# Optimization experiments

Hardware: AMD Instinct MI355X
Metric: run time of the kernel (lower is better)

Reference implementation:

```python
import jax, jax.numpy as jnp
import numpy as np

B, T, V, NS, L, G, H = 16, 256, 18000, 30, 10, 3, 400


def setup_inputs() -> dict:
    key = jax.random.key(0)
    ks = jax.random.split(key, 12)
    return {
        'encoded_hidden': jax.random.normal(ks[0], (1, B, H), jnp.float32),
        'encoded_outputs': jax.random.normal(ks[1], (B, T, H), jnp.float32),
        'emb_weight': jax.random.normal(ks[2], (V, H), jnp.float32) * 0.02,
        'gru_w_ih': jax.random.normal(ks[3], (3 * H, H), jnp.float32) * 0.05,
        'gru_w_hh': jax.random.normal(ks[4], (3 * H, H), jnp.float32) * 0.05,
        'gru_b_ih': jnp.zeros((3 * H,), jnp.float32),
        'gru_b_hh': jnp.zeros((3 * H,), jnp.float32),
        'w_ratio': jax.random.normal(ks[5], (1, 3 * H), jnp.float32) * 0.05,
        'b_ratio': jnp.zeros((1,), jnp.float32),
        'w_gate': jax.random.normal(ks[6], (G, H), jnp.float32) * 0.05,
        'b_gate': jnp.zeros((G,), jnp.float32),
        'slot_emb': jax.random.normal(ks[7], (2 * NS, H), jnp.float32) * 0.1,
        'encoded_lens': jax.random.randint(ks[8], (B,), T // 2, T + 1, jnp.int32),
        'story': jax.random.randint(ks[9], (B, T), 0, V, jnp.int32),
        'target_batches': jax.random.randint(ks[10], (B, NS, L), 0, V, jnp.int32),
        'domain_idx': 2 * jnp.arange(NS, dtype=jnp.int32),
        'slotname_idx': 2 * jnp.arange(NS, dtype=jnp.int32) + 1,
    }


def _forward(encoded_hidden, encoded_outputs, emb_weight, gru_w_ih, gru_w_hh,
             gru_b_ih, gru_b_hh, w_ratio, b_ratio, w_gate, b_gate, slot_emb,
             encoded_lens, story, target_batches, domain_idx, slotname_idx):
    b, t, h = encoded_outputs.shape
    ns, l = target_batches.shape[1], target_batches.shape[2]
    n = ns * b  # flattened slot-major rows: row = slot*b + batch

    combined = slot_emb[domain_idx] + slot_emb[slotname_idx]          # (NS,H)
    dec_in0 = jnp.repeat(combined, b, axis=0)                          # (N,H)
    h0 = jnp.tile(encoded_hidden[0], (ns, 1))                          # (N,H)
    enc = jnp.tile(encoded_outputs, (ns, 1, 1))                        # (N,T,H)
    story_rep = jnp.tile(story, (ns, 1))                               # (N,T)
    lens_rep = jnp.tile(encoded_lens, ns)                              # (N,)
    mask = jnp.arange(t)[None, :] < lens_rep[:, None]                  # (N,T)
    rows = jnp.arange(n)[:, None]

    # teacher forcing: decoder input at step wi>=1 is emb of target at wi-1
    tgt = jnp.transpose(target_batches, (2, 1, 0)).reshape(l, n)       # (L,N)
    dec_inputs = jnp.concatenate([dec_in0[None], emb_weight[tgt[:-1]]], axis=0)

    def step(hid, x):
        gi = x @ gru_w_ih.T + gru_b_ih
        gh = hid @ gru_w_hh.T + gru_b_hh
        i_r, i_z, i_n = jnp.split(gi, 3, axis=-1)
        h_r, h_z, h_n = jnp.split(gh, 3, axis=-1)
        r = jax.nn.sigmoid(i_r + h_r)
        z = jax.nn.sigmoid(i_z + h_z)
        nn_ = jnp.tanh(i_n + r * h_n)
        h_new = (1.0 - z) * nn_ + z * hid                              # (N,H)
        # attend over encoder outputs
        scores = jnp.einsum('nh,nth->nt', h_new, enc)
        scores = jnp.where(mask, scores, -1e9)
        prob = jax.nn.softmax(scores, axis=1)                          # (N,T)
        context = jnp.einsum('nt,nth->nh', prob, enc)                  # (N,H)
        # vocab distribution
        p_vocab = jax.nn.softmax(h_new @ emb_weight.T, axis=1)         # (N,V)
        # pointer-generator mix
        p_gen_vec = jnp.concatenate([h_new, context, x], axis=-1)      # (N,3H)
        switch = jax.nn.sigmoid(p_gen_vec @ w_ratio.T + b_ratio)       # (N,1)
        p_ctx = jnp.zeros_like(p_vocab).at[rows, story_rep].add(prob)  # scatter-add
        final = (1.0 - switch) * p_ctx + switch * p_vocab              # (N,V)
        return h_new, (final, context)

    _, (finals, contexts) = jax.lax.scan(step, h0, dec_inputs)
    points = finals.reshape(l, ns, b, -1).transpose(1, 2, 0, 3)        # (NS,B,L,V)
    gates = (contexts[0] @ w_gate.T + b_gate).reshape(ns, b, -1)       # (NS,B,G)
    return points, gates


def reference(encoded_hidden, encoded_outputs, emb_weight, gru_w_ih, gru_w_hh,
              gru_b_ih, gru_b_hh, w_ratio, b_ratio, w_gate, b_gate, slot_emb,
              encoded_lens, story, target_batches, domain_idx, slotname_idx):
    return _forward(encoded_hidden, encoded_outputs, emb_weight, gru_w_ih,
                    gru_w_hh, gru_b_ih, gru_b_hh, w_ratio, b_ratio, w_gate,
                    b_gate, slot_emb, encoded_lens, story, target_batches,
                    domain_idx, slotname_idx)
```

## Files before the change

kernel.cpp:

```cpp
#include <hip/hip_runtime.h>
#include <hip/hip_bf16.h>

#define Bq 16
#define Tq 256
#define Vq 18000
#define NSq 30
#define Lq 10
#define Gq 3
#define Hq 400
#define Nq (NSq * Bq)
#define H3q (3 * Hq)
#define NKT 25
#define NGV 564
#define NGW 38
#define NGH 15
#define NPB 288
#define NPB_USED 282
#define NGHB 152

typedef __bf16 bf16;
typedef __bf16 bf16x4 __attribute__((ext_vector_type(4)));
typedef __bf16 bf16x8 __attribute__((ext_vector_type(8)));
typedef float floatx16 __attribute__((ext_vector_type(16)));

__global__ __launch_bounds__(256) void k_f2b4(
    const float* __restrict__ src, bf16* __restrict__ dst, const int n4)
{
    int i = blockIdx.x * 256 + threadIdx.x;
    if (i >= n4) return;
    const float4 v = ((const float4*)src)[i];
    bf16x4 o;
    o[0] = (bf16)v.x; o[1] = (bf16)v.y; o[2] = (bf16)v.z; o[3] = (bf16)v.w;
    ((bf16x4*)dst)[i] = o;
}

__global__ __launch_bounds__(256) void k_enct(
    const bf16* __restrict__ encb, bf16* __restrict__ encT)
{
    const int b = blockIdx.x;
    const int k0 = blockIdx.y * 32;
    const int t = threadIdx.x;
    const bf16* src = encb + ((size_t)(b * Tq + t)) * Hq + k0;
    #pragma unroll
    for (int j = 0; j < 32; ++j) {
        if (k0 + j < Hq)
            encT[((size_t)b * Hq + k0 + j) * Tq + t] = src[j];
    }
}

__global__ __launch_bounds__(256) void k_packf(
    const float* __restrict__ src, bf16* __restrict__ dst,
    const int ngroups, const int nrows)
{
    const int i = blockIdx.x * 256 + threadIdx.x;
    if (i >= ngroups * NKT * 64) return;
    const int lane = i & 63;
    const int kt = (i >> 6) % NKT;
    const int g = i / (NKT * 64);
    int row = g * 32 + (lane & 31);
    if (row >= nrows) row = nrows - 1;
    const int k0 = kt * 16 + (lane >> 5) * 8;
    const float* s = src + (size_t)row * Hq + k0;
    const float4 a = *(const float4*)s;
    const float4 c = *(const float4*)(s + 4);
    bf16x8 o;
    o[0] = (bf16)a.x; o[1] = (bf16)a.y; o[2] = (bf16)a.z; o[3] = (bf16)a.w;
    o[4] = (bf16)c.x; o[5] = (bf16)c.y; o[6] = (bf16)c.z; o[7] = (bf16)c.w;
    *(bf16x8*)(dst + (size_t)i * 8) = o;
}

__global__ __launch_bounds__(256) void k_xball(
    const float* __restrict__ slot_emb, const int* __restrict__ dom,
    const int* __restrict__ slo, const float* __restrict__ emb,
    const int* __restrict__ tgt, bf16* __restrict__ xbp,
    bf16* __restrict__ xlin)
{
    const int i = blockIdx.x * 256 + threadIdx.x;
    if (i >= Lq * NGH * NKT * 64) return;
    const int lane = i & 63;
    const int kt = (i >> 6) % NKT;
    const int gg = i / (NKT * 64);
    const int g = gg % NGH;
    const int s = gg / NGH;
    const int n = g * 32 + (lane & 31);
    const int slot = n >> 4, b = n & (Bq - 1);
    const int k0 = kt * 16 + (lane >> 5) * 8;
    float v[8];
    if (s == 0) {
        const float* p1 = slot_emb + (size_t)dom[slot] * Hq + k0;
        const float* p2 = slot_emb + (size_t)slo[slot] * Hq + k0;
        #pragma unroll
        for (int j = 0; j < 8; ++j) v[j] = p1[j] + p2[j];
    } else {
        const int tv = tgt[(b * NSq + slot) * Lq + (s - 1)];
        const float* p = emb + (size_t)tv * Hq + k0;
        #pragma unroll
        for (int j = 0; j < 8; ++j) v[j] = p[j];
    }
    bf16x8 o;
    #pragma unroll
    for (int j = 0; j < 8; ++j) o[j] = (bf16)v[j];
    *(bf16x8*)(xbp + (size_t)i * 8) = o;
    *(bf16x8*)(xlin + ((size_t)(s * Nq + n)) * Hq + k0) = o;
}

__global__ __launch_bounds__(256) void k_h0(
    const float* __restrict__ ehid, float* __restrict__ h,
    bf16* __restrict__ hbp)
{
    const int i = blockIdx.x * 256 + threadIdx.x;
    if (i >= NGH * NKT * 64) return;
    const int lane = i & 63;
    const int kt = (i >> 6) % NKT;
    const int g = i / (NKT * 64);
    const int n = g * 32 + (lane & 31);
    const int b = n & (Bq - 1);
    const int k0 = kt * 16 + (lane >> 5) * 8;
    const float* s = ehid + (size_t)b * Hq + k0;
    bf16x8 o;
    #pragma unroll
    for (int j = 0; j < 8; ++j) {
        float v = s[j];
        h[(size_t)n * Hq + k0 + j] = v;
        o[j] = (bf16)v;
    }
    *(bf16x8*)(hbp + (size_t)i * 8) = o;
}

__global__ __launch_bounds__(256) void k_gi_all(
    const bf16* __restrict__ xbp, const bf16* __restrict__ wihp,
    float* __restrict__ gi_all)
{
    const int ct = blockIdx.x;
    const int s = blockIdx.y;
    const int wave = threadIdx.x >> 6, lane = threadIdx.x & 63;
    floatx16 acc[4];
    #pragma unroll
    for (int i = 0; i < 4; ++i)
        #pragma unroll
        for (int r = 0; r < 16; ++r) acc[i][r] = 0.f;
    for (int kt = 0; kt < NKT; ++kt) {
        const bf16x8 w = *(const bf16x8*)(wihp + ((size_t)(ct * NKT + kt) * 64 + lane) * 8);
        #pragma unroll
        for (int i = 0; i < 4; ++i) {
            const int g = wave + 4 * i;
            if (g < NGH) {
                const bf16x8 a = *(const bf16x8*)(xbp +
                    ((size_t)((s * NGH + g) * NKT + kt) * 64 + lane) * 8);
                acc[i] = __builtin_amdgcn_mfma_f32_32x32x16_bf16(a, w, acc[i], 0, 0, 0);
            }
        }
    }
    const int j = ct * 32 + (lane & 31);
    if (j >= H3q) return;
    #pragma unroll
    for (int i = 0; i < 4; ++i) {
        const int g = wave + 4 * i;
        if (g < NGH) {
            const int rbase = g * 32 + 4 * (lane >> 5);
            #pragma unroll
            for (int r = 0; r < 16; ++r) {
                const int rr = rbase + (r & 3) + 8 * (r >> 2);
                gi_all[((size_t)(s * Nq + rr)) * H3q + j] = acc[i][r];
            }
        }
    }
}

__global__ __launch_bounds__(256) void k_gh(
    const bf16* __restrict__ hbp, const bf16* __restrict__ whhp,
    float* __restrict__ gh)
{
    const int ct = blockIdx.x;
    const int wave = threadIdx.x >> 6, lane = threadIdx.x & 63;
    const int g = blockIdx.y * 4 + wave;
    if (g >= NGH) return;
    floatx16 acc;
    #pragma unroll
    for (int r = 0; r < 16; ++r) acc[r] = 0.f;
    for (int kt = 0; kt < NKT; ++kt) {
        const bf16x8 a = *(const bf16x8*)(hbp + ((size_t)(g * NKT + kt) * 64 + lane) * 8);
        const bf16x8 w = *(const bf16x8*)(whhp + ((size_t)(ct * NKT + kt) * 64 + lane) * 8);
        acc = __builtin_amdgcn_mfma_f32_32x32x16_bf16(a, w, acc, 0, 0, 0);
    }
    const int j = ct * 32 + (lane & 31);
    if (j >= H3q) return;
    const int rbase = g * 32 + 4 * (lane >> 5);
    #pragma unroll
    for (int r = 0; r < 16; ++r) {
        const int rr = rbase + (r & 3) + 8 * (r >> 2);
        gh[(size_t)rr * H3q + j] = acc[r];
    }
}

__global__ __launch_bounds__(256) void k_fused(
    const int n_attn, const int step_a, const int step_f,
    const float* __restrict__ gi_all, const float* __restrict__ gh,
    const float* __restrict__ b_ih, const float* __restrict__ b_hh,
    float* __restrict__ h, bf16* __restrict__ hbp,
    const bf16* __restrict__ xlin, const bf16* __restrict__ encb,
    const bf16* __restrict__ encT, const int* __restrict__ lens,
    const float* __restrict__ w_ratio, const float* __restrict__ b_ratio,
    const float* __restrict__ w_gate, const float* __restrict__ b_gate,
    float* __restrict__ prob_a, float* __restrict__ swp_a,
    float* __restrict__ out_gates,
    const bf16* __restrict__ eLb, const float* __restrict__ prob_f,
    const float* __restrict__ swp_f, const float* __restrict__ partial,
    const int* __restrict__ story, float* __restrict__ out)
{
    __shared__ float s_h[Hq];
    __shared__ float s_c[Hq];
    __shared__ float s_p[Tq];
    __shared__ float s_red[8];
    const int tid = threadIdx.x;

    if ((int)blockIdx.x >= n_attn) {
        const int n = blockIdx.x - n_attn;
        const int b = n & (Bq - 1);

        float ps = 0.f;
        if (tid < NPB_USED) ps = partial[(size_t)n * NPB + tid];
        if (tid < NPB_USED - 256) ps += partial[(size_t)n * NPB + 256 + tid];
        #pragma unroll
        for (int off = 32; off > 0; off >>= 1) ps += __shfl_xor(ps, off, 64);
        if ((tid & 63) == 0) s_red[tid >> 6] = ps;
        __syncthreads();
        const float rs = s_red[0] + s_red[1] + s_red[2] + s_red[3];
        const float swv = swp_f[n];
        const float scale = swv / rs;

        const bf16* er = eLb + (size_t)n * Vq;
        float* orow = out + ((size_t)n * Lq + step_f) * Vq;
        for (int i8 = tid; i8 < Vq / 8; i8 += 256) {
            const bf16x8 e = *(const bf16x8*)(er + i8 * 8);
            float4 o0, o1;
            o0.x = (float)e[0] * scale; o0.y = (float)e[1] * scale;
            o0.z = (float)e[2] * scale; o0.w = (float)e[3] * scale;
            o1.x = (float)e[4] * scale; o1.y = (float)e[5] * scale;
            o1.z = (float)e[6] * scale; o1.w = (float)e[7] * scale;
            ((float4*)orow)[i8 * 2]     = o0;
            ((float4*)orow)[i8 * 2 + 1] = o1;
        }
        __syncthreads();
        __threadfence_block();
        const int idx = story[b * Tq + tid];
        atomicAdd(orow + idx, (1.f - swv) * prob_f[(size_t)n * Tq + tid]);
        return;
    }

    const int n = blockIdx.x;
    const int b = n & (Bq - 1);

    const float* gin = gi_all + ((size_t)step_a * Nq + n) * H3q;
    const float* ghn = gh + (size_t)n * H3q;
    for (int k = tid; k < Hq; k += 256) {
        float ir = gin[k]          + b_ih[k];
        float hr = ghn[k]          + b_hh[k];
        float iz = gin[Hq + k]     + b_ih[Hq + k];
        float hz = ghn[Hq + k]     + b_hh[Hq + k];
        float in_ = gin[2*Hq + k]  + b_ih[2*Hq + k];
        float hn_ = ghn[2*Hq + k]  + b_hh[2*Hq + k];
        float r = 1.f / (1.f + __expf(-(ir + hr)));
        float z = 1.f / (1.f + __expf(-(iz + hz)));
        float nn = tanhf(in_ + r * hn_);
        float hp = h[(size_t)n * Hq + k];
        float hv = (1.f - z) * nn + z * hp;
        s_h[k] = hv;
        h[(size_t)n * Hq + k] = hv;
        hbp[((size_t)(((n >> 5) * NKT + (k >> 4)) * 64
                      + ((k >> 3) & 1) * 32 + (n & 31))) * 8 + (k & 7)] = (bf16)hv;
    }
    __syncthreads();

    const int t = tid;
    const bf16* ecT = encT + (size_t)b * Hq * Tq + t;
    float sc = 0.f;
    #pragma unroll 8
    for (int k = 0; k < Hq; ++k)
        sc += s_h[k] * (float)ecT[(size_t)k * Tq];
    const int len = lens[b];
    float score = (t < len) ? sc : -1e9f;

    float mx = score;
    for (int off = 32; off > 0; off >>= 1) mx = fmaxf(mx, __shfl_xor(mx, off, 64));
    if ((tid & 63) == 0) s_red[tid >> 6] = mx;
    __syncthreads();
    mx = fmaxf(fmaxf(s_red[0], s_red[1]), fmaxf(s_red[2], s_red[3]));
    float ev = __expf(score - mx);
    float sm = ev;
    for (int off = 32; off > 0; off >>= 1) sm += __shfl_xor(sm, off, 64);
    __syncthreads();
    if ((tid & 63) == 0) s_red[tid >> 6] = sm;
    __syncthreads();
    sm = s_red[0] + s_red[1] + s_red[2] + s_red[3];
    float p = ev / sm;
    s_p[t] = p;
    prob_a[(size_t)n * Tq + t] = p;
    __syncthreads();

    for (int k = tid; k < Hq; k += 256) {
        float c = 0.f;
        const bf16* ecol = encb + (size_t)b * Tq * Hq + k;
        for (int tt = 0; tt < Tq; ++tt) c += s_p[tt] * (float)ecol[(size_t)tt * Hq];
        s_c[k] = c;
    }
    __syncthreads();

    const bf16* xr = xlin + ((size_t)step_a * Nq + n) * Hq;
    float part2 = 0.f;
    for (int k = tid; k < Hq; k += 256) {
        part2 += w_ratio[k]        * s_h[k]
               + w_ratio[Hq + k]   * s_c[k]
               + w_ratio[2*Hq + k] * (float)xr[k];
    }
    for (int off = 32; off > 0; off >>= 1) part2 += __shfl_xor(part2, off, 64);
    __syncthreads();
    if ((tid & 63) == 0) s_red[tid >> 6] = part2;
    __syncthreads();
    if (tid == 0) {
        float tot = s_red[0] + s_red[1] + s_red[2] + s_red[3] + b_ratio[0];
        swp_a[n] = 1.f / (1.f + __expf(-tot));
    }

    if (step_a == 0) {
        for (int gg = 0; gg < Gq; ++gg) {
            float pg = 0.f;
            for (int k = tid; k < Hq; k += 256)
                pg += w_gate[gg * Hq + k] * s_c[k];
            for (int off = 32; off > 0; off >>= 1) pg += __shfl_xor(pg, off, 64);
            __syncthreads();
            if ((tid & 63) == 0) s_red[tid >> 6] = pg;
            __syncthreads();
            if (tid == 0)
                out_gates[n * Gq + gg] =
                    s_red[0] + s_red[1] + s_red[2] + s_red[3] + b_gate[gg];
        }
    }
}

__global__ __launch_bounds__(256, 2) void k_vocab_gh(
    const bf16* __restrict__ hbp, const bf16* __restrict__ embp,
    const bf16* __restrict__ whhp, bf16* __restrict__ eLb,
    float* __restrict__ partial, float* __restrict__ gh)
{
    const int wave = threadIdx.x >> 6, lane = threadIdx.x & 63;

    if (blockIdx.x >= NPB_USED) {
        const int bid2 = blockIdx.x - NPB_USED;
        const int ct = bid2 % NGW;
        const int g = (bid2 / NGW) * 4 + wave;
        if (g >= NGH) return;
        floatx16 acc;
        #pragma unroll
        for (int r = 0; r < 16; ++r) acc[r] = 0.f;
        for (int kt = 0; kt < NKT; ++kt) {
            const bf16x8 a = *(const bf16x8*)(hbp + ((size_t)(g * NKT + kt) * 64 + lane) * 8);
            const bf16x8 w = *(const bf16x8*)(whhp + ((size_t)(ct * NKT + kt) * 64 + lane) * 8);
            acc = __builtin_amdgcn_mfma_f32_32x32x16_bf16(a, w, acc, 0, 0, 0);
        }
        const int j = ct * 32 + (lane & 31);
        if (j >= H3q) return;
        const int rbase = g * 32 + 4 * (lane >> 5);
        #pragma unroll
        for (int r = 0; r < 16; ++r) {
            const int rr = rbase + (r & 3) + 8 * (r >> 2);
            gh[(size_t)rr * H3q + j] = acc[r];
        }
        return;
    }

    const int ct2 = blockIdx.x;
    floatx16 acc0[4], acc1[4];
    #pragma unroll
    for (int i = 0; i < 4; ++i)
        #pragma unroll
        for (int r = 0; r < 16; ++r) { acc0[i][r] = 0.f; acc1[i][r] = 0.f; }

    for (int kt = 0; kt < NKT; ++kt) {
        const bf16x8 w0 = *(const bf16x8*)(embp +
            ((size_t)((2 * ct2) * NKT + kt) * 64 + lane) * 8);
        const bf16x8 w1 = *(const bf16x8*)(embp +
            ((size_t)((2 * ct2 + 1) * NKT + kt) * 64 + lane) * 8);
        #pragma unroll
        for (int i = 0; i < 4; ++i) {
            const int g = wave + 4 * i;
            if (g < NGH) {
                const bf16x8 a = *(const bf16x8*)(hbp +
                    ((size_t)(g * NKT + kt) * 64 + lane) * 8);
                acc0[i] = __builtin_amdgcn_mfma_f32_32x32x16_bf16(a, w0, acc0[i], 0, 0, 0);
                acc1[i] = __builtin_amdgcn_mfma_f32_32x32x16_bf16(a, w1, acc1[i], 0, 0, 0);
            }
        }
    }

    const int mcol = lane & 31, half = lane >> 5;
    const int j0 = ct2 * 64 + mcol, j1 = j0 + 32;
    #pragma unroll
    for (int i = 0; i < 4; ++i) {
        const int g = wave + 4 * i;
        if (g >= NGH) continue;
        const int rbase = g * 32 + 4 * half;
        #pragma unroll
        for (int r = 0; r < 16; ++r) {
            const int rr = rbase + (r & 3) + 8 * (r >> 2);
            const float e0 = (j0 < Vq) ? __expf(acc0[i][r]) : 0.f;
            const float e1 = (j1 < Vq) ? __expf(acc1[i][r]) : 0.f;
            if (j0 < Vq) eLb[(size_t)rr * Vq + j0] = (bf16)e0;
            if (j1 < Vq) eLb[(size_t)rr * Vq + j1] = (bf16)e1;
            float v = e0 + e1;
            v += __shfl_xor(v, 16, 64);
            v += __shfl_xor(v, 8, 64);
            v += __shfl_xor(v, 4, 64);
            v += __shfl_xor(v, 2, 64);
            v += __shfl_xor(v, 1, 64);
            if (mcol == 0) partial[(size_t)rr * NPB + ct2] = v;
        }
    }
}

extern "C" void kernel_launch(void* const* d_in, const int* in_sizes, int n_in,
                              void* d_out, int out_size, void* d_ws, size_t ws_size,
                              hipStream_t stream)
{
    const float* ehid    = (const float*)d_in[0];
    const float* enc     = (const float*)d_in[1];
    const float* emb     = (const float*)d_in[2];
    const float* w_ih    = (const float*)d_in[3];
    const float* w_hh    = (const float*)d_in[4];
    const float* b_ih    = (const float*)d_in[5];
    const float* b_hh    = (const float*)d_in[6];
    const float* w_ratio = (const float*)d_in[7];
    const float* b_ratio = (const float*)d_in[8];
    const float* w_gate  = (const float*)d_in[9];
    const float* b_gate  = (const float*)d_in[10];
    const float* slot_emb= (const float*)d_in[11];
    const int*  lens     = (const int*)d_in[12];
    const int*  story    = (const int*)d_in[13];
    const int*  tgt      = (const int*)d_in[14];
    const int*  dom      = (const int*)d_in[15];
    const int*  slo      = (const int*)d_in[16];

    float* out = (float*)d_out;
    float* out_gates = out + (size_t)NSq * Bq * Lq * Vq;

    char* w = (char*)d_ws;
    size_t off = 0;
    auto alloc = [&](size_t bytes) -> void* {
        void* p = (void*)(w + off);
        off += (bytes + 255) & ~(size_t)255;
        return p;
    };
    bf16*  xbp    = (bf16*)alloc((size_t)Lq * Nq * Hq * 2);
    bf16*  xlin   = (bf16*)alloc((size_t)Lq * Nq * Hq * 2);
    bf16*  hbp    = (bf16*)alloc((size_t)Nq * Hq * 2);
    float* h      = (float*)alloc((size_t)Nq * Hq * 4);
    float* gi_all = (float*)alloc((size_t)Lq * Nq * H3q * 4);
    float* gh     = (float*)alloc((size_t)Nq * H3q * 4);
    float* prob0  = (float*)alloc((size_t)Nq * Tq * 4);
    float* prob1  = (float*)alloc((size_t)Nq * Tq * 4);
    float* swp0   = (float*)alloc((size_t)Nq * 4);
    float* swp1   = (float*)alloc((size_t)Nq * 4);
    float* partial= (float*)alloc((size_t)Nq * NPB * 4);
    bf16*  eLb    = (bf16*)alloc((size_t)Nq * Vq * 2);
    bf16*  embp   = (bf16*)alloc((size_t)NGV * NKT * 64 * 8 * 2);
    bf16*  wihp   = (bf16*)alloc((size_t)NGW * NKT * 64 * 8 * 2);
    bf16*  whhp   = (bf16*)alloc((size_t)NGW * NKT * 64 * 8 * 2);
    bf16*  encb   = (bf16*)alloc((size_t)Bq * Tq * Hq * 2);
    bf16*  encT   = (bf16*)alloc((size_t)Bq * Hq * Tq * 2);

    {
        int nf;
        nf = NGV * NKT * 64;
        k_packf<<<dim3((nf + 255) / 256), dim3(256), 0, stream>>>(emb, embp, NGV, Vq);
        nf = NGW * NKT * 64;
        k_packf<<<dim3((nf + 255) / 256), dim3(256), 0, stream>>>(w_ih, wihp, NGW, H3q);
        k_packf<<<dim3((nf + 255) / 256), dim3(256), 0, stream>>>(w_hh, whhp, NGW, H3q);
        const int n4 = (Bq * Tq * Hq) / 4;
        k_f2b4<<<dim3((n4 + 255) / 256), dim3(256), 0, stream>>>(enc, encb, n4);
        k_enct<<<dim3(Bq, 13), dim3(256), 0, stream>>>(encb, encT);
        nf = Lq * NGH * NKT * 64;
        k_xball<<<dim3((nf + 255) / 256), dim3(256), 0, stream>>>(
            slot_emb, dom, slo, emb, tgt, xbp, xlin);
        nf = NGH * NKT * 64;
        k_h0<<<dim3((nf + 255) / 256), dim3(256), 0, stream>>>(ehid, h, hbp);
        k_gi_all<<<dim3(NGW, Lq), dim3(256), 0, stream>>>(xbp, wihp, gi_all);
        k_gh<<<dim3(NGW, 4), dim3(256), 0, stream>>>(hbp, whhp, gh);
    }

    k_fused<<<dim3(Nq), dim3(256), 0, stream>>>(
        Nq, 0, 0, gi_all, gh, b_ih, b_hh, h, hbp, xlin, encb, encT, lens,
        w_ratio, b_ratio, w_gate, b_gate, prob0, swp0, out_gates,
        eLb, prob1, swp1, partial, story, out);

    for (int s = 0; s < Lq; ++s) {
        const int nb = NPB_USED + ((s + 1 < Lq) ? NGHB : 0);
        k_vocab_gh<<<dim3(nb), dim3(256), 0, stream>>>(
            hbp, embp, whhp, eLb, partial, gh);
        const int na = (s + 1 < Lq) ? Nq : 0;
        float* pa = ((s + 1) & 1) ? prob1 : prob0;
        float* sa = ((s + 1) & 1) ? swp1 : swp0;
        const float* pf = (s & 1) ? prob1 : prob0;
        const float* sf = (s & 1) ? swp1 : swp0;
        k_fused<<<dim3(na + Nq), dim3(256), 0, stream>>>(
            na, s + 1, s, gi_all, gh, b_ih, b_hh, h, hbp, xlin, encb, encT,
            lens, w_ratio, b_ratio, w_gate, b_gate, pa, sa, out_gates,
            eLb, pf, sf, partial, story, out);
    }
}
```

Measured before the change: 1.326 ms.

## Fuse prep kernels, drop encT transpose, scatter-add in LDS before writing output rows

Merges the preprocessing kernels (weight packing, enc conversion, input gathering, h0 init) into one grid-stride kernel, and merges the gi_all and initial gh GEMMs into a single launch. It removes the encT transpose, so attention scores now read encb rows with vector loads. The output-finalize path now builds each vocab row in LDS in two 9000-element chunks, applies the pointer scatter-add with shared-memory atomics, and then streams the row out, replacing global atomics that followed a full row write. This cuts launch count and global atomic traffic, at the cost of a large LDS footprint per block that may lower occupancy.

```diff
diff --git a/kernel.cpp b/kernel.cpp
--- a/kernel.cpp
+++ b/kernel.cpp
@@ -14,46 +14,20 @@
 #define NGV 564
 #define NGW 38
 #define NGH 15
+#define CHq 9000
 #define NPB 288
 #define NPB_USED 282
-#define NGHB 152
+#define NGT 152
+#define NGI 380
 
 typedef __bf16 bf16;
 typedef __bf16 bf16x4 __attribute__((ext_vector_type(4)));
 typedef __bf16 bf16x8 __attribute__((ext_vector_type(8)));
 typedef float floatx16 __attribute__((ext_vector_type(16)));
 
-__global__ __launch_bounds__(256) void k_f2b4(
-    const float* __restrict__ src, bf16* __restrict__ dst, const int n4)
-{
-    int i = blockIdx.x * 256 + threadIdx.x;
-    if (i >= n4) return;
-    const float4 v = ((const float4*)src)[i];
-    bf16x4 o;
-    o[0] = (bf16)v.x; o[1] = (bf16)v.y; o[2] = (bf16)v.z; o[3] = (bf16)v.w;
-    ((bf16x4*)dst)[i] = o;
-}
-
-__global__ __launch_bounds__(256) void k_enct(
-    const bf16* __restrict__ encb, bf16* __restrict__ encT)
-{
-    const int b = blockIdx.x;
-    const int k0 = blockIdx.y * 32;
-    const int t = threadIdx.x;
-    const bf16* src = encb + ((size_t)(b * Tq + t)) * Hq + k0;
-    #pragma unroll
-    for (int j = 0; j < 32; ++j) {
-        if (k0 + j < Hq)
-            encT[((size_t)b * Hq + k0 + j) * Tq + t] = src[j];
-    }
-}
-
-__global__ __launch_bounds__(256) void k_packf(
-    const float* __restrict__ src, bf16* __restrict__ dst,
-    const int ngroups, const int nrows)
-{
-    const int i = blockIdx.x * 256 + threadIdx.x;
-    if (i >= ngroups * NKT * 64) return;
+__device__ __forceinline__ void packf_one(const float* __restrict__ src,
+    bf16* __restrict__ dst, const int i, const int nrows)
+{
     const int lane = i & 63;
     const int kt = (i >> 6) % NKT;
     const int g = i / (NKT * 64);
@@ -69,71 +43,115 @@
     *(bf16x8*)(dst + (size_t)i * 8) = o;
 }
 
-__global__ __launch_bounds__(256) void k_xball(
+__global__ __launch_bounds__(256) void k_p0(
+    const float* __restrict__ emb, const float* __restrict__ w_ih,
+    const float* __restrict__ w_hh, const float* __restrict__ enc,
     const float* __restrict__ slot_emb, const int* __restrict__ dom,
-    const int* __restrict__ slo, const float* __restrict__ emb,
-    const int* __restrict__ tgt, bf16* __restrict__ xbp,
-    bf16* __restrict__ xlin)
-{
-    const int i = blockIdx.x * 256 + threadIdx.x;
-    if (i >= Lq * NGH * NKT * 64) return;
-    const int lane = i & 63;
-    const int kt = (i >> 6) % NKT;
-    const int gg = i / (NKT * 64);
-    const int g = gg % NGH;
-    const int s = gg / NGH;
-    const int n = g * 32 + (lane & 31);
-    const int slot = n >> 4, b = n & (Bq - 1);
-    const int k0 = kt * 16 + (lane >> 5) * 8;
-    float v[8];
-    if (s == 0) {
-        const float* p1 = slot_emb + (size_t)dom[slot] * Hq + k0;
-        const float* p2 = slot_emb + (size_t)slo[slot] * Hq + k0;
-        #pragma unroll
-        for (int j = 0; j < 8; ++j) v[j] = p1[j] + p2[j];
-    } else {
-        const int tv = tgt[(b * NSq + slot) * Lq + (s - 1)];
-        const float* p = emb + (size_t)tv * Hq + k0;
-        #pragma unroll
-        for (int j = 0; j < 8; ++j) v[j] = p[j];
-    }
-    bf16x8 o;
-    #pragma unroll
-    for (int j = 0; j < 8; ++j) o[j] = (bf16)v[j];
-    *(bf16x8*)(xbp + (size_t)i * 8) = o;
-    *(bf16x8*)(xlin + ((size_t)(s * Nq + n)) * Hq + k0) = o;
-}
-
-__global__ __launch_bounds__(256) void k_h0(
-    const float* __restrict__ ehid, float* __restrict__ h,
-    bf16* __restrict__ hbp)
-{
-    const int i = blockIdx.x * 256 + threadIdx.x;
-    if (i >= NGH * NKT * 64) return;
-    const int lane = i & 63;
-    const int kt = (i >> 6) % NKT;
-    const int g = i / (NKT * 64);
-    const int n = g * 32 + (lane & 31);
-    const int b = n & (Bq - 1);
-    const int k0 = kt * 16 + (lane >> 5) * 8;
-    const float* s = ehid + (size_t)b * Hq + k0;
-    bf16x8 o;
-    #pragma unroll
-    for (int j = 0; j < 8; ++j) {
-        float v = s[j];
-        h[(size_t)n * Hq + k0 + j] = v;
-        o[j] = (bf16)v;
-    }
-    *(bf16x8*)(hbp + (size_t)i * 8) = o;
-}
-
-__global__ __launch_bounds__(256) void k_gi_all(
+    const int* __restrict__ slo, const int* __restrict__ tgt,
+    const float* __restrict__ ehid,
+    bf16* __restrict__ embp, bf16* __restrict__ wihp, bf16* __restrict__ whhp,
+    bf16* __restrict__ encb, bf16* __restrict__ xbp, bf16* __restrict__ xlin,
+    float* __restrict__ h, bf16* __restrict__ hbp)
+{
+    const int gtid = blockIdx.x * 256 + threadIdx.x;
+    const int GT = gridDim.x * 256;
+
+    for (int i = gtid; i < NGV * NKT * 64; i += GT)
+        packf_one(emb, embp, i, Vq);
+    for (int i = gtid; i < NGW * NKT * 64; i += GT) {
+        packf_one(w_ih, wihp, i, H3q);
+        packf_one(w_hh, whhp, i, H3q);
+    }
+    for (int i = gtid; i < (Bq * Tq * Hq) / 4; i += GT) {
+        const float4 v = ((const float4*)enc)[i];
+        bf16x4 o;
+        o[0] = (bf16)v.x; o[1] = (bf16)v.y; o[2] = (bf16)v.z; o[3] = (bf16)v.w;
+        ((bf16x4*)encb)[i] = o;
+    }
+    for (int i = gtid; i < Lq * NGH * NKT * 64; i += GT) {
+        const int lane = i & 63;
+        const int kt = (i >> 6) % NKT;
+        const int gg = i / (NKT * 64);
+        const int g = gg % NGH;
+        const int s = gg / NGH;
+        const int n = g * 32 + (lane & 31);
+        const int slot = n >> 4, b = n & (Bq - 1);
+        const int k0 = kt * 16 + (lane >> 5) * 8;
+        float v[8];
+        if (s == 0) {
+            const float* p1 = slot_emb + (size_t)dom[slot] * Hq + k0;
+            const float* p2 = slot_emb + (size_t)slo[slot] * Hq + k0;
+            #pragma unroll
+            for (int j = 0; j < 8; ++j) v[j] = p1[j] + p2[j];
+        } else {
+            const int tv = tgt[(b * NSq + slot) * Lq + (s - 1)];
+            const float* q = emb + (size_t)tv * Hq + k0;
+            #pragma unroll
+            for (int j = 0; j < 8; ++j) v[j] = q[j];
+        }
+        bf16x8 o;
+        #pragma unroll
+        for (int j = 0; j < 8; ++j) o[j] = (bf16)v[j];
+        *(bf16x8*)(xbp + (size_t)i * 8) = o;
+        *(bf16x8*)(xlin + ((size_t)s * Nq + n) * Hq + k0) = o;
+    }
+    for (int i = gtid; i < NGH * NKT * 64; i += GT) {
+        const int lane = i & 63;
+        const int kt = (i >> 6) % NKT;
+        const int g = i / (NKT * 64);
+        const int n = g * 32 + (lane & 31);
+        const int b = n & (Bq - 1);
+        const int k0 = kt * 16 + (lane >> 5) * 8;
+        const float* s = ehid + (size_t)b * Hq + k0;
+        bf16x8 o;
+        #pragma unroll
+        for (int j = 0; j < 8; ++j) {
+            const float v = s[j];
+            h[(size_t)n * Hq + k0 + j] = v;
+            o[j] = (bf16)v;
+        }
+        *(bf16x8*)(hbp + (size_t)i * 8) = o;
+    }
+}
+
+__device__ __forceinline__ void gh_unit(const bf16* __restrict__ hbp,
+    const bf16* __restrict__ whhp, float* __restrict__ gh, const int v,
+    const int wave, const int lane)
+{
+    const int ct = v % NGW;
+    const int g = (v / NGW) * 4 + wave;
+    if (g >= NGH) return;
+    floatx16 acc;
+    #pragma unroll
+    for (int r = 0; r < 16; ++r) acc[r] = 0.f;
+    for (int kt = 0; kt < NKT; ++kt) {
+        const bf16x8 a = *(const bf16x8*)(hbp + ((size_t)(g * NKT + kt) * 64 + lane) * 8);
+        const bf16x8 w = *(const bf16x8*)(whhp + ((size_t)(ct * NKT + kt) * 64 + lane) * 8);
+        acc = __builtin_amdgcn_mfma_f32_32x32x16_bf16(a, w, acc, 0, 0, 0);
+    }
+    const int j = ct * 32 + (lane & 31);
+    if (j >= H3q) return;
+    const int rbase = g * 32 + 4 * (lane >> 5);
+    #pragma unroll
+    for (int r = 0; r < 16; ++r) {
+        const int rr = rbase + (r & 3) + 8 * (r >> 2);
+        gh[(size_t)rr * H3q + j] = acc[r];
+    }
+}
+
+__global__ __launch_bounds__(256) void k_p1(
     const bf16* __restrict__ xbp, const bf16* __restrict__ wihp,
-    float* __restrict__ gi_all)
-{
-    const int ct = blockIdx.x;
-    const int s = blockIdx.y;
+    const bf16* __restrict__ hbp, const bf16* __restrict__ whhp,
+    float* __restrict__ gi_all, float* __restrict__ gh)
+{
     const int wave = threadIdx.x >> 6, lane = threadIdx.x & 63;
+    const int u = blockIdx.x;
+    if (u >= NGI) {
+        gh_unit(hbp, whhp, gh, u - NGI, wave, lane);
+        return;
+    }
+    const int ct = u % NGW;
+    const int s = u / NGW;
     floatx16 acc[4];
     #pragma unroll
     for (int i = 0; i < 4; ++i)
@@ -167,91 +185,21 @@
     }
 }
 
-__global__ __launch_bounds__(256) void k_gh(
-    const bf16* __restrict__ hbp, const bf16* __restrict__ whhp,
-    float* __restrict__ gh)
-{
-    const int ct = blockIdx.x;
-    const int wave = threadIdx.x >> 6, lane = threadIdx.x & 63;
-    const int g = blockIdx.y * 4 + wave;
-    if (g >= NGH) return;
-    floatx16 acc;
-    #pragma unroll
-    for (int r = 0; r < 16; ++r) acc[r] = 0.f;
-    for (int kt = 0; kt < NKT; ++kt) {
-        const bf16x8 a = *(const bf16x8*)(hbp + ((size_t)(g * NKT + kt) * 64 + lane) * 8);
-        const bf16x8 w = *(const bf16x8*)(whhp + ((size_t)(ct * NKT + kt) * 64 + lane) * 8);
-        acc = __builtin_amdgcn_mfma_f32_32x32x16_bf16(a, w, acc, 0, 0, 0);
-    }
-    const int j = ct * 32 + (lane & 31);
-    if (j >= H3q) return;
-    const int rbase = g * 32 + 4 * (lane >> 5);
-    #pragma unroll
-    for (int r = 0; r < 16; ++r) {
-        const int rr = rbase + (r & 3) + 8 * (r >> 2);
-        gh[(size_t)rr * H3q + j] = acc[r];
-    }
-}
-
-__global__ __launch_bounds__(256) void k_fused(
-    const int n_attn, const int step_a, const int step_f,
+__device__ void attn_row(const int n, const int step,
     const float* __restrict__ gi_all, const float* __restrict__ gh,
     const float* __restrict__ b_ih, const float* __restrict__ b_hh,
     float* __restrict__ h, bf16* __restrict__ hbp,
     const bf16* __restrict__ xlin, const bf16* __restrict__ encb,
-    const bf16* __restrict__ encT, const int* __restrict__ lens,
-    const float* __restrict__ w_ratio, const float* __restrict__ b_ratio,
-    const float* __restrict__ w_gate, const float* __restrict__ b_gate,
-    float* __restrict__ prob_a, float* __restrict__ swp_a,
-    float* __restrict__ out_gates,
-    const bf16* __restrict__ eLb, const float* __restrict__ prob_f,
-    const float* __restrict__ swp_f, const float* __restrict__ partial,
-    const int* __restrict__ story, float* __restrict__ out)
-{
-    __shared__ float s_h[Hq];
-    __shared__ float s_c[Hq];
-    __shared__ float s_p[Tq];
-    __shared__ float s_red[8];
+    const int* __restrict__ lens, const float* __restrict__ w_ratio,
+    const float* __restrict__ b_ratio, const float* __restrict__ w_gate,
+    const float* __restrict__ b_gate, float* __restrict__ prob_a,
+    float* __restrict__ swp_a, float* __restrict__ out_gates,
+    float* s_h, float* s_c, float* s_p, float* s_red)
+{
+    const int b = n & (Bq - 1);
     const int tid = threadIdx.x;
 
-    if ((int)blockIdx.x >= n_attn) {
-        const int n = blockIdx.x - n_attn;
-        const int b = n & (Bq - 1);
-
-        float ps = 0.f;
-        if (tid < NPB_USED) ps = partial[(size_t)n * NPB + tid];
-        if (tid < NPB_USED - 256) ps += partial[(size_t)n * NPB + 256 + tid];
-        #pragma unroll
-        for (int off = 32; off > 0; off >>= 1) ps += __shfl_xor(ps, off, 64);
-        if ((tid & 63) == 0) s_red[tid >> 6] = ps;
-        __syncthreads();
-        const float rs = s_red[0] + s_red[1] + s_red[2] + s_red[3];
-        const float swv = swp_f[n];
-        const float scale = swv / rs;
-
-        const bf16* er = eLb + (size_t)n * Vq;
-        float* orow = out + ((size_t)n * Lq + step_f) * Vq;
-        for (int i8 = tid; i8 < Vq / 8; i8 += 256) {
-            const bf16x8 e = *(const bf16x8*)(er + i8 * 8);
-            float4 o0, o1;
-            o0.x = (float)e[0] * scale; o0.y = (float)e[1] * scale;
-            o0.z = (float)e[2] * scale; o0.w = (float)e[3] * scale;
-            o1.x = (float)e[4] * scale; o1.y = (float)e[5] * scale;
-            o1.z = (float)e[6] * scale; o1.w = (float)e[7] * scale;
-            ((float4*)orow)[i8 * 2]     = o0;
-            ((float4*)orow)[i8 * 2 + 1] = o1;
-        }
-        __syncthreads();
-        __threadfence_block();
-        const int idx = story[b * Tq + tid];
-        atomicAdd(orow + idx, (1.f - swv) * prob_f[(size_t)n * Tq + tid]);
-        return;
-    }
-
-    const int n = blockIdx.x;
-    const int b = n & (Bq - 1);
-
-    const float* gin = gi_all + ((size_t)step_a * Nq + n) * H3q;
+    const float* gin = gi_all + ((size_t)step * Nq + n) * H3q;
     const float* ghn = gh + (size_t)n * H3q;
     for (int k = tid; k < Hq; k += 256) {
         float ir = gin[k]          + b_ih[k];
@@ -273,11 +221,14 @@
     __syncthreads();
 
     const int t = tid;
-    const bf16* ecT = encT + (size_t)b * Hq * Tq + t;
+    const bf16* erow = encb + (size_t)(b * Tq + t) * Hq;
     float sc = 0.f;
-    #pragma unroll 8
-    for (int k = 0; k < Hq; ++k)
-        sc += s_h[k] * (float)ecT[(size_t)k * Tq];
+    #pragma unroll 5
+    for (int kc = 0; kc < Hq / 8; ++kc) {
+        const bf16x8 e = *(const bf16x8*)(erow + kc * 8);
+        #pragma unroll
+        for (int j = 0; j < 8; ++j) sc += s_h[kc * 8 + j] * (float)e[j];
+    }
     const int len = lens[b];
     float score = (t < len) ? sc : -1e9f;
 
@@ -293,9 +244,9 @@
     if ((tid & 63) == 0) s_red[tid >> 6] = sm;
     __syncthreads();
     sm = s_red[0] + s_red[1] + s_red[2] + s_red[3];
-    float p = ev / sm;
-    s_p[t] = p;
-    prob_a[(size_t)n * Tq + t] = p;
+    const float pv = ev / sm;
+    s_p[t] = pv;
+    prob_a[(size_t)n * Tq + t] = pv;
     __syncthreads();
 
     for (int k = tid; k < Hq; k += 256) {
@@ -306,7 +257,7 @@
     }
     __syncthreads();
 
-    const bf16* xr = xlin + ((size_t)step_a * Nq + n) * Hq;
+    const bf16* xr = xlin + ((size_t)step * Nq + n) * Hq;
     float part2 = 0.f;
     for (int k = tid; k < Hq; k += 256) {
         part2 += w_ratio[k]        * s_h[k]
@@ -318,11 +269,11 @@
     if ((tid & 63) == 0) s_red[tid >> 6] = part2;
     __syncthreads();
     if (tid == 0) {
-        float tot = s_red[0] + s_red[1] + s_red[2] + s_red[3] + b_ratio[0];
+        const float tot = s_red[0] + s_red[1] + s_red[2] + s_red[3] + b_ratio[0];
         swp_a[n] = 1.f / (1.f + __expf(-tot));
     }
 
-    if (step_a == 0) {
+    if (step == 0) {
         for (int gg = 0; gg < Gq; ++gg) {
             float pg = 0.f;
             for (int k = tid; k < Hq; k += 256)
@@ -338,7 +289,24 @@
     }
 }
 
-__global__ __launch_bounds__(256, 2) void k_vocab_gh(
+__global__ __launch_bounds__(256) void k_attn0(
+    const float* __restrict__ gi_all, const float* __restrict__ gh,
+    const float* __restrict__ b_ih, const float* __restrict__ b_hh,
+    float* __restrict__ h, bf16* __restrict__ hbp,
+    const bf16* __restrict__ xlin, const bf16* __restrict__ encb,
+    const int* __restrict__ lens, const float* __restrict__ w_ratio,
+    const float* __restrict__ b_ratio, const float* __restrict__ w_gate,
+    const float* __restrict__ b_gate, float* __restrict__ prob0,
+    float* __restrict__ swp0, float* __restrict__ out_gates)
+{
+    __shared__ float smem[2 * Hq + Tq];
+    __shared__ float s_red[8];
+    attn_row(blockIdx.x, 0, gi_all, gh, b_ih, b_hh, h, hbp, xlin, encb, lens,
+             w_ratio, b_ratio, w_gate, b_gate, prob0, swp0, out_gates,
+             smem, smem + Hq, smem + 2 * Hq, s_red);
+}
+
+__global__ __launch_bounds__(256, 2) void k_A(
     const bf16* __restrict__ hbp, const bf16* __restrict__ embp,
     const bf16* __restrict__ whhp, bf16* __restrict__ eLb,
     float* __restrict__ partial, float* __restrict__ gh)
@@ -346,26 +314,7 @@
     const int wave = threadIdx.x >> 6, lane = threadIdx.x & 63;
 
     if (blockIdx.x >= NPB_USED) {
-        const int bid2 = blockIdx.x - NPB_USED;
-        const int ct = bid2 % NGW;
-        const int g = (bid2 / NGW) * 4 + wave;
-        if (g >= NGH) return;
-        floatx16 acc;
-        #pragma unroll
-        for (int r = 0; r < 16; ++r) acc[r] = 0.f;
-        for (int kt = 0; kt < NKT; ++kt) {
-            const bf16x8 a = *(const bf16x8*)(hbp + ((size_t)(g * NKT + kt) * 64 + lane) * 8);
-            const bf16x8 w = *(const bf16x8*)(whhp + ((size_t)(ct * NKT + kt) * 64 + lane) * 8);
-            acc = __builtin_amdgcn_mfma_f32_32x32x16_bf16(a, w, acc, 0, 0, 0);
-        }
-        const int j = ct * 32 + (lane & 31);
-        if (j >= H3q) return;
-        const int rbase = g * 32 + 4 * (lane >> 5);
-        #pragma unroll
-        for (int r = 0; r < 16; ++r) {
-            const int rr = rbase + (r & 3) + 8 * (r >> 2);
-            gh[(size_t)rr * H3q + j] = acc[r];
-        }
+        gh_unit(hbp, whhp, gh, blockIdx.x - NPB_USED, wave, lane);
         return;
     }
 
@@ -415,6 +364,74 @@
             v += __shfl_xor(v, 1, 64);
             if (mcol == 0) partial[(size_t)rr * NPB + ct2] = v;
         }
+    }
+}
+
+__global__ __launch_bounds__(256) void k_B(
+    const int step_f,
+    const float* __restrict__ gi_all, const float* __restrict__ gh,
+    const float* __restrict__ b_ih, const float* __restrict__ b_hh,
+    float* __restrict__ h, bf16* __restrict__ hbp,
+    const bf16* __restrict__ xlin, const bf16* __restrict__ encb,
+    const int* __restrict__ lens, const float* __restrict__ w_ratio,
+    const float* __restrict__ b_ratio, const float* __restrict__ w_gate,
+    const float* __restrict__ b_gate, float* __restrict__ prob_a,
+    float* __restrict__ swp_a, float* __restrict__ out_gates,
+    const bf16* __restrict__ eLb, const float* __restrict__ prob_f,
+    const float* __restrict__ swp_f, const float* __restrict__ partial,
+    const int* __restrict__ story, float* __restrict__ out)
+{
+    __shared__ __align__(16) float smem[CHq];
+    __shared__ float s_red[8];
+    const int tid = threadIdx.x;
+
+    if ((int)blockIdx.x >= Nq) {
+        attn_row(blockIdx.x - Nq, step_f + 1, gi_all, gh, b_ih, b_hh, h, hbp,
+                 xlin, encb, lens, w_ratio, b_ratio, w_gate, b_gate,
+                 prob_a, swp_a, out_gates,
+                 smem, smem + Hq, smem + 2 * Hq, s_red);
+        return;
+    }
+
+    const int n = blockIdx.x;
+    const int b = n & (Bq - 1);
+
+    float ps = partial[(size_t)n * NPB + tid];
+    if (tid < NPB_USED - 256) ps += partial[(size_t)n * NPB + 256 + tid];
+    #pragma unroll
+    for (int off = 32; off > 0; off >>= 1) ps += __shfl_xor(ps, off, 64);
+    if ((tid & 63) == 0) s_red[tid >> 6] = ps;
+    __syncthreads();
+    const float rs = s_red[0] + s_red[1] + s_red[2] + s_red[3];
+    const float swv = swp_f[n];
+    const float scale = swv / rs;
+
+    const bf16* er = eLb + (size_t)n * Vq;
+    float* orow = out + ((size_t)n * Lq + step_f) * Vq;
+
+    #pragma unroll
+    for (int c = 0; c < 2; ++c) {
+        const int c0 = c * CHq;
+        for (int i8 = tid; i8 < CHq / 8; i8 += 256) {
+            const bf16x8 e = *(const bf16x8*)(er + c0 + i8 * 8);
+            float4 o0, o1;
+            o0.x = (float)e[0] * scale; o0.y = (float)e[1] * scale;
+            o0.z = (float)e[2] * scale; o0.w = (float)e[3] * scale;
+            o1.x = (float)e[4] * scale; o1.y = (float)e[5] * scale;
+            o1.z = (float)e[6] * scale; o1.w = (float)e[7] * scale;
+            ((float4*)smem)[i8 * 2]     = o0;
+            ((float4*)smem)[i8 * 2 + 1] = o1;
+        }
+        __syncthreads();
+        {
+            const int idx = story[b * Tq + tid];
+            if (idx >= c0 && idx < c0 + CHq)
+                atomicAdd(&smem[idx - c0], (1.f - swv) * prob_f[(size_t)n * Tq + tid]);
+        }
+        __syncthreads();
+        for (int i4 = tid; i4 < CHq / 4; i4 += 256)
+            ((float4*)(orow + c0))[i4] = ((const float4*)smem)[i4];
+        if (c == 0) __syncthreads();
     }
 }
 
@@ -446,9 +463,9 @@
     char* w = (char*)d_ws;
     size_t off = 0;
     auto alloc = [&](size_t bytes) -> void* {
-        void* p = (void*)(w + off);
+        void* q = (void*)(w + off);
         off += (bytes + 255) & ~(size_t)255;
-        return p;
+        return q;
     };
     bf16*  xbp    = (bf16*)alloc((size_t)Lq * Nq * Hq * 2);
     bf16*  xlin   = (bf16*)alloc((size_t)Lq * Nq * Hq * 2);
@@ -466,44 +483,29 @@
     bf16*  wihp   = (bf16*)alloc((size_t)NGW * NKT * 64 * 8 * 2);
     bf16*  whhp   = (bf16*)alloc((size_t)NGW * NKT * 64 * 8 * 2);
     bf16*  encb   = (bf16*)alloc((size_t)Bq * Tq * Hq * 2);
-    bf16*  encT   = (bf16*)alloc((size_t)Bq * Hq * Tq * 2);
-
-    {
-        int nf;
-        nf = NGV * NKT * 64;
-        k_packf<<<dim3((nf + 255) / 256), dim3(256), 0, stream>>>(emb, embp, NGV, Vq);
-        nf = NGW * NKT * 64;
-        k_packf<<<dim3((nf + 255) / 256), dim3(256), 0, stream>>>(w_ih, wihp, NGW, H3q);
-        k_packf<<<dim3((nf + 255) / 256), dim3(256), 0, stream>>>(w_hh, whhp, NGW, H3q);
-        const int n4 = (Bq * Tq * Hq) / 4;
-        k_f2b4<<<dim3((n4 + 255) / 256), dim3(256), 0, stream>>>(enc, encb, n4);
-        k_enct<<<dim3(Bq, 13), dim3(256), 0, stream>>>(encb, encT);
-        nf = Lq * NGH * NKT * 64;
-        k_xball<<<dim3((nf + 255) / 256), dim3(256), 0, stream>>>(
-            slot_emb, dom, slo, emb, tgt, xbp, xlin);
-        nf = NGH * NKT * 64;
-        k_h0<<<dim3((nf + 255) / 256), dim3(256), 0, stream>>>(ehid, h, hbp);
-        k_gi_all<<<dim3(NGW, Lq), dim3(256), 0, stream>>>(xbp, wihp, gi_all);
-        k_gh<<<dim3(NGW, 4), dim3(256), 0, stream>>>(hbp, whhp, gh);
-    }
-
-    k_fused<<<dim3(Nq), dim3(256), 0, stream>>>(
-        Nq, 0, 0, gi_all, gh, b_ih, b_hh, h, hbp, xlin, encb, encT, lens,
-        w_ratio, b_ratio, w_gate, b_gate, prob0, swp0, out_gates,
-        eLb, prob1, swp1, partial, story, out);
+
+    k_p0<<<dim3(2048), dim3(256), 0, stream>>>(
+        emb, w_ih, w_hh, enc, slot_emb, dom, slo, tgt, ehid,
+        embp, wihp, whhp, encb, xbp, xlin, h, hbp);
+    k_p1<<<dim3(NGI + NGT), dim3(256), 0, stream>>>(
+        xbp, wihp, hbp, whhp, gi_all, gh);
+    k_attn0<<<dim3(Nq), dim3(256), 0, stream>>>(
+        gi_all, gh, b_ih, b_hh, h, hbp, xlin, encb, lens,
+        w_ratio, b_ratio, w_gate, b_gate, prob0, swp0, out_gates);
 
     for (int s = 0; s < Lq; ++s) {
-        const int nb = NPB_USED + ((s + 1 < Lq) ? NGHB : 0);
-        k_vocab_gh<<<dim3(nb), dim3(256), 0, stream>>>(
+        const int nbA = NPB_USED + ((s + 1 < Lq) ? NGT : 0);
+        k_A<<<dim3(nbA), dim3(256), 0, stream>>>(
             hbp, embp, whhp, eLb, partial, gh);
-        const int na = (s + 1 < Lq) ? Nq : 0;
+
+        const int nbB = Nq + ((s + 1 < Lq) ? Nq : 0);
         float* pa = ((s + 1) & 1) ? prob1 : prob0;
         float* sa = ((s + 1) & 1) ? swp1 : swp0;
         const float* pf = (s & 1) ? prob1 : prob0;
         const float* sf = (s & 1) ? swp1 : swp0;
-        k_fused<<<dim3(na + Nq), dim3(256), 0, stream>>>(
-            na, s + 1, s, gi_all, gh, b_ih, b_hh, h, hbp, xlin, encb, encT,
-            lens, w_ratio, b_ratio, w_gate, b_gate, pa, sa, out_gates,
+        k_B<<<dim3(nbB), dim3(256), 0, stream>>>(
+            s, gi_all, gh, b_ih, b_hh, h, hbp, xlin, encb, lens,
+            w_ratio, b_ratio, w_gate, b_gate, pa, sa, out_gates,
             eLb, pf, sf, partial, story, out);
     }
 }
```

New measurement: 1.203 ms. 9.3% less time.
